# Kernel optimization log

Hardware: AMD Instinct MI355X
Metric: run time of the kernel (lower is better)

Reference implementation:

```python
import jax, jax.numpy as jnp
import numpy as np
from jax import lax

SFREQ = 250.0
ORDER = 4
BANDS = [(4.0, 8.0), (8.0, 12.0), (12.0, 16.0), (16.0, 20.0), (20.0, 24.0), (24.0, 28.0), (28.0, 32.0), (32.0, 36.0), (36.0, 40.0)]
KLEN = int(SFREQ // 2)
if KLEN % 2 == 0:
    KLEN += 1  # 125 taps, odd -> same-length output with pad K//2


def _butter_bandpass(order, low, high, sfreq):
    # numpy reimplementation of scipy.signal.butter(order, [low,high]/nyq, btype='band')
    nyq = sfreq / 2.0
    fs = 2.0
    warped = 2.0 * fs * np.tan(np.pi * np.array([low, high]) / nyq / fs)
    m = np.arange(-order + 1, order, 2)
    p = -np.exp(1j * np.pi * m / (2 * order))  # analog Butterworth LP prototype poles
    k = 1.0
    bw = warped[1] - warped[0]
    wo = np.sqrt(warped[0] * warped[1])
    p_lp = p * bw / 2.0
    p_bp = np.concatenate([p_lp + np.sqrt(p_lp ** 2 - wo ** 2), p_lp - np.sqrt(p_lp ** 2 - wo ** 2)])
    z_bp = np.zeros(order, dtype=complex)
    k_bp = k * bw ** order
    fs2 = 2.0 * fs  # bilinear transform
    z_d = (fs2 + z_bp) / (fs2 - z_bp)
    p_d = (fs2 + p_bp) / (fs2 - p_bp)
    z_d = np.append(z_d, -np.ones(len(p_bp) - len(z_bp)))
    k_d = k_bp * np.real(np.prod(fs2 - z_bp) / np.prod(fs2 - p_bp))
    b = np.real(k_d * np.poly(z_d))
    a = np.real(np.poly(p_d))
    return b, a


def _make_kernel(low, high):
    # IIR impulse response (centered impulse, as in the torch module), Hann window, L1 normalize
    b, a = _butter_bandpass(ORDER, low, high, SFREQ)
    x = np.zeros(KLEN)
    x[KLEN // 2] = 1.0
    h = np.zeros(KLEN)
    for n in range(KLEN):
        s = 0.0
        for i in range(len(b)):
            if n - i >= 0:
                s += b[i] * x[n - i]
        for j in range(1, len(a)):
            if n - j >= 0:
                s -= a[j] * h[n - j]
        h[n] = s / a[0]
    nn = np.arange(KLEN)
    h = h * (0.5 - 0.5 * np.cos(2.0 * np.pi * nn / (KLEN - 1)))  # symmetric Hann
    return h / np.sum(np.abs(h))


def setup_inputs() -> dict:
    key = jax.random.key(0)
    x = jax.random.normal(key, (64, 64, 1000), dtype=jnp.float32)  # (B, C, T) EEG
    kernels = jnp.asarray(np.stack([_make_kernel(lo, hi) for lo, hi in BANDS]), dtype=jnp.float32)  # (n_bands, K)
    return {"x": x, "kernels": kernels}


def reference(x, kernels):
    # out[b, i, c, t] = cross-correlation of channel c with band-i kernel (torch Conv1d semantics)
    B, C, T = x.shape
    nb, K = kernels.shape
    pad = K // 2
    x2 = x.reshape(B * C, 1, T)
    w = kernels[:, None, :]  # (n_bands, 1, K)
    y = lax.conv_general_dilated(x2, w, (1,), [(pad, pad)], dimension_numbers=("NCH", "OIH", "NCH"))
    return y.reshape(B, C, nb, T).transpose(0, 2, 1, 3)  # (B, n_bands, C, T)
```

## Files before the change

### kernel.cpp

```cpp
#include <hip/hip_runtime.h>
#include <hip/hip_bf16.h>


#define T_LEN    1000
#define NB       9
#define KP       128
#define S_COPY   1160
#define SLOTS    145

typedef __attribute__((ext_vector_type(8))) short short8;
typedef __attribute__((ext_vector_type(4))) float f32x4;

__device__ __forceinline__ unsigned int f2bf(float f) {
    union { __hip_bfloat16 h; unsigned short u; } cv;
    cv.h = __float2bfloat16(f);
    return (unsigned int)cv.u;
}

__global__ __launch_bounds__(256) void prep_taps(const float* __restrict__ kern,
                                                 unsigned short* __restrict__ kwb) {
    const int t = threadIdx.x;
    #pragma unroll
    for (int i = 0; i < 8; ++i) {
        int idx = t + 256 * i;
        int band = idx >> 7, k = idx & 127;
        float v = (band < NB && k < 125) ? kern[band * 125 + k] : 0.f;
        kwb[idx] = (unsigned short)f2bf(v);
    }
}

__global__ __launch_bounds__(256) void fbank_mfma(
    const float* __restrict__ x,
    const unsigned short* __restrict__ kwb,
    float* __restrict__ out)
{
    __shared__ unsigned short xs[8 * S_COPY];

    const int tid = threadIdx.x;
    const int bc  = blockIdx.x;
    const int b   = bc >> 6, c = bc & 63;
    const float* xrow = x + (size_t)bc * T_LEN;

    {
        const int r = tid >> 5, q0 = tid & 31;
        #pragma unroll
        for (int i = 0; i < 5; ++i) {
            int q = q0 + 32 * i;
            if (q < SLOTS) {
                int idx0 = 8 * q + r - 64;
                unsigned int d[4];
                #pragma unroll
                for (int e2 = 0; e2 < 4; ++e2) {
                    int i0 = idx0 + 2 * e2, i1 = i0 + 1;
                    float v0 = ((unsigned)i0 < T_LEN) ? xrow[i0] : 0.f;
                    float v1 = ((unsigned)i1 < T_LEN) ? xrow[i1] : 0.f;
                    d[e2] = f2bf(v0) | (f2bf(v1) << 16);
                }
                *reinterpret_cast<uint4*>(&xs[r * S_COPY + 8 * q]) =
                    make_uint4(d[0], d[1], d[2], d[3]);
            }
        }
    }

    const int lane = tid & 63;
    const int wid  = tid >> 6;
    const int j = lane & 15, g = lane >> 4;
    short8 a[4];
    #pragma unroll
    for (int kk = 0; kk < 4; ++kk)
        a[kk] = *reinterpret_cast<const short8*>(kwb + j * KP + kk * 32 + g * 8);

    __syncthreads();

    const int t0w = wid << 8;
    const int rl  = (j + 2) & 7;
    const char* xsb = reinterpret_cast<const char*>(xs);
    const int LB = 2 * (1159 * rl + 2 + j + 8 * g + t0w);

    float* obase = out + ((size_t)b * NB * 64 + c) * T_LEN + t0w + j;
    const int tj = t0w + j;

    short8 w[8];
    #pragma unroll
    for (int m = 0; m < 6; ++m)
        w[m] = *reinterpret_cast<const short8*>(xsb + LB + 32 * m);

    #pragma unroll
    for (int p = 0; p < 8; ++p) {
        w[(2 * p + 6) & 7] = *reinterpret_cast<const short8*>(xsb + LB + 32 * (2 * p + 6));
        w[(2 * p + 7) & 7] = *reinterpret_cast<const short8*>(xsb + LB + 32 * (2 * p + 7));
        f32x4 ae = {0.f, 0.f, 0.f, 0.f}, ao = {0.f, 0.f, 0.f, 0.f};
        #pragma unroll
        for (int kk = 0; kk < 4; ++kk) {
            ae = __builtin_amdgcn_mfma_f32_16x16x32_bf16(a[kk], w[(2 * p + 2 * kk) & 7], ae, 0, 0, 0);
            ao = __builtin_amdgcn_mfma_f32_16x16x32_bf16(a[kk], w[(2 * p + 1 + 2 * kk) & 7], ao, 0, 0, 0);
        }
        const int te = 32 * p, to = te + 16;
        #pragma unroll
        for (int reg = 0; reg < 4; ++reg) {
            int band = 4 * g + reg;
            if (band < NB) {
                if (tj + te < T_LEN) obase[(size_t)band * 64000 + te] = ae[reg];
                if (tj + to < T_LEN) obase[(size_t)band * 64000 + to] = ao[reg];
            }
        }
    }
}

extern "C" void kernel_launch(void* const* d_in, const int* in_sizes, int n_in,
                              void* d_out, int out_size, void* d_ws, size_t ws_size,
                              hipStream_t stream) {
    const float* x    = (const float*)d_in[0];
    const float* kern = (const float*)d_in[1];
    float* out = (float*)d_out;
    unsigned short* kwb = (unsigned short*)d_ws;

    prep_taps<<<1, 256, 0, stream>>>(kern, kwb);
    fbank_mfma<<<64 * 64, 256, 0, stream>>>(x, kwb, out);
}
```

Before: 53.50 us.

## Transpose MFMA operands for vectorized nontemporal stores and drop tap prep kernel

Swaps the MFMA A/B operands so each lane's accumulator holds four consecutive time samples of one band, which allows a single 16-byte nontemporal store per lane instead of scattered scalar stores. The separate tap-conversion kernel is removed and each thread converts its own taps from fp32 to bf16 inside the main kernel, saving a launch. Launch bounds now request 5 blocks per SM. The cost is redundant tap loads and conversions in every block.

```diff
diff --git a/kernel.cpp b/kernel.cpp
--- a/kernel.cpp
+++ b/kernel.cpp
@@ -4,7 +4,6 @@
 
 #define T_LEN    1000
 #define NB       9
-#define KP       128
 #define S_COPY   1160
 #define SLOTS    145
 
@@ -17,21 +16,9 @@
     return (unsigned int)cv.u;
 }
 
-__global__ __launch_bounds__(256) void prep_taps(const float* __restrict__ kern,
-                                                 unsigned short* __restrict__ kwb) {
-    const int t = threadIdx.x;
-    #pragma unroll
-    for (int i = 0; i < 8; ++i) {
-        int idx = t + 256 * i;
-        int band = idx >> 7, k = idx & 127;
-        float v = (band < NB && k < 125) ? kern[band * 125 + k] : 0.f;
-        kwb[idx] = (unsigned short)f2bf(v);
-    }
-}
-
-__global__ __launch_bounds__(256) void fbank_mfma(
+__global__ __launch_bounds__(256, 5) void fbank_mfma(
     const float* __restrict__ x,
-    const unsigned short* __restrict__ kwb,
+    const float* __restrict__ kern,
     float* __restrict__ out)
 {
     __shared__ unsigned short xs[8 * S_COPY];
@@ -64,46 +51,49 @@
 
     const int lane = tid & 63;
     const int wid  = tid >> 6;
-    const int j = lane & 15, g = lane >> 4;
-    short8 a[4];
+    const int n = lane & 15, g = lane >> 4;
+
+    short8 bt[4];
     #pragma unroll
-    for (int kk = 0; kk < 4; ++kk)
-        a[kk] = *reinterpret_cast<const short8*>(kwb + j * KP + kk * 32 + g * 8);
+    for (int kk = 0; kk < 4; ++kk) {
+        unsigned int u[4];
+        #pragma unroll
+        for (int e2 = 0; e2 < 4; ++e2) {
+            int k0 = kk * 32 + 8 * g + 2 * e2;
+            float v0 = (n < NB && k0 < 125)     ? kern[n * 125 + k0]     : 0.f;
+            float v1 = (n < NB && k0 + 1 < 125) ? kern[n * 125 + k0 + 1] : 0.f;
+            u[e2] = f2bf(v0) | (f2bf(v1) << 16);
+        }
+        union { uint4 u4; short8 s8; } cv;
+        cv.u4 = make_uint4(u[0], u[1], u[2], u[3]);
+        bt[kk] = cv.s8;
+    }
 
     __syncthreads();
 
     const int t0w = wid << 8;
-    const int rl  = (j + 2) & 7;
+    const int rl  = (n + 2) & 7;
     const char* xsb = reinterpret_cast<const char*>(xs);
-    const int LB = 2 * (1159 * rl + 2 + j + 8 * g + t0w);
+    const int LB = 2 * (1159 * rl + 2 + n + 8 * g + t0w);
 
-    float* obase = out + ((size_t)b * NB * 64 + c) * T_LEN + t0w + j;
-    const int tj = t0w + j;
+    short8 F[8];
+    #pragma unroll
+    for (int u = 0; u < 6; ++u)
+        F[u] = *reinterpret_cast<const short8*>(xsb + LB + 32 * u);
 
-    short8 w[8];
-    #pragma unroll
-    for (int m = 0; m < 6; ++m)
-        w[m] = *reinterpret_cast<const short8*>(xsb + LB + 32 * m);
+    const bool bandok = (n < NB);
+    float* obase = out + ((size_t)(b * NB + n) * 64 + c) * T_LEN + t0w + 4 * g;
 
     #pragma unroll
-    for (int p = 0; p < 8; ++p) {
-        w[(2 * p + 6) & 7] = *reinterpret_cast<const short8*>(xsb + LB + 32 * (2 * p + 6));
-        w[(2 * p + 7) & 7] = *reinterpret_cast<const short8*>(xsb + LB + 32 * (2 * p + 7));
-        f32x4 ae = {0.f, 0.f, 0.f, 0.f}, ao = {0.f, 0.f, 0.f, 0.f};
+    for (int m = 0; m < 16; ++m) {
+        F[(m + 6) & 7] = *reinterpret_cast<const short8*>(xsb + LB + 32 * (m + 6));
+        f32x4 acc = {0.f, 0.f, 0.f, 0.f};
         #pragma unroll
-        for (int kk = 0; kk < 4; ++kk) {
-            ae = __builtin_amdgcn_mfma_f32_16x16x32_bf16(a[kk], w[(2 * p + 2 * kk) & 7], ae, 0, 0, 0);
-            ao = __builtin_amdgcn_mfma_f32_16x16x32_bf16(a[kk], w[(2 * p + 1 + 2 * kk) & 7], ao, 0, 0, 0);
-        }
-        const int te = 32 * p, to = te + 16;
-        #pragma unroll
-        for (int reg = 0; reg < 4; ++reg) {
-            int band = 4 * g + reg;
-            if (band < NB) {
-                if (tj + te < T_LEN) obase[(size_t)band * 64000 + te] = ae[reg];
-                if (tj + to < T_LEN) obase[(size_t)band * 64000 + to] = ao[reg];
-            }
-        }
+        for (int kk = 0; kk < 4; ++kk)
+            acc = __builtin_amdgcn_mfma_f32_16x16x32_bf16(F[(m + 2 * kk) & 7], bt[kk], acc, 0, 0, 0);
+        const int t4 = t0w + 16 * m + 4 * g;
+        if (bandok && t4 + 4 <= T_LEN)
+            __builtin_nontemporal_store(acc, reinterpret_cast<f32x4*>(obase + 16 * m));
     }
 }
 
@@ -113,8 +103,6 @@
     const float* x    = (const float*)d_in[0];
     const float* kern = (const float*)d_in[1];
     float* out = (float*)d_out;
-    unsigned short* kwb = (unsigned short*)d_ws;
 
-    prep_taps<<<1, 256, 0, stream>>>(kern, kwb);
-    fbank_mfma<<<64 * 64, 256, 0, stream>>>(x, kwb, out);
+    fbank_mfma<<<64 * 64, 256, 0, stream>>>(x, kern, out);
 }
```

New measurement: 96.91 us. +81.1%, slower.
